# Performance work log

Measured on AMD Instinct MI355X. Metric: run time of the kernel, lower is better.

## Reference

```python
import jax, jax.numpy as jnp
import numpy as np

H = 8          # num_head
HD = 64        # head_dim = hidden_dim // num_head
WIN = 33       # atten_window_size (odd)
MIN_SCORE = -1e9


def setup_inputs() -> dict:
    key = jax.random.key(0)
    ks = jax.random.split(key, 12)
    B, S, D = 8, 4096, 512
    scale = 1.0 / np.sqrt(D).astype(np.float32)

    def lin_w(k):
        return jax.random.normal(k, (D, D), jnp.float32) * scale

    return {
        "query": jax.random.normal(ks[0], (B, S, D), jnp.float32),
        "key": jax.random.normal(ks[1], (B, S, D), jnp.float32),
        "value": jax.random.normal(ks[2], (B, S, D), jnp.float32),
        "mask": jax.random.randint(ks[3], (B, S), 0, 2).astype(bool),
        "Wq": lin_w(ks[4]), "bq": jax.random.normal(ks[5], (D,), jnp.float32) * 0.02,
        "Wk": lin_w(ks[6]), "bk": jax.random.normal(ks[7], (D,), jnp.float32) * 0.02,
        "Wv": lin_w(ks[8]), "bv": jax.random.normal(ks[9], (D,), jnp.float32) * 0.02,
        "Wo": lin_w(ks[10]), "bo": jax.random.normal(ks[11], (D,), jnp.float32) * 0.02,
    }


def reference(query, key, value, mask, Wq, bq, Wk, bk, Wv, bv, Wo, bo):
    B, S, D = query.shape
    half = min(WIN // 2, S // 2)

    def proj_split(x, W, b):
        # nn.Linear: x @ W.T + b; then split heads and flatten (B,H) -> B*H
        y = x @ W.T + b
        return y.reshape(B, S, H, HD).transpose(0, 2, 1, 3).reshape(B * H, S, HD)

    q = proj_split(query, Wq, bq)   # [BH, S, HD]
    k = proj_split(key, Wk, bk)
    v = proj_split(value, Wv, bv)
    # mask expanded over heads; True = masked (LocalAttention semantics)
    m = jnp.broadcast_to(mask[:, None, :], (B, H, S)).reshape(B * H, S)

    # banded scores: one [BH, S] vector per window offset (no sqrt(head_dim) scaling,
    # faithful to LocalAttention)
    scores = []
    for off in range(-half, half + 1):
        if off < 0:
            w = jnp.sum(q[:, -off:] * k[:, :off], axis=-1)
            w = jnp.where(m[:, :off], MIN_SCORE, w)
            w = jnp.pad(w, ((0, 0), (-off, 0)), constant_values=MIN_SCORE)
        elif off == 0:
            w = jnp.where(m, MIN_SCORE, jnp.sum(q * k, axis=-1))
        else:
            w = jnp.sum(q[:, :-off] * k[:, off:], axis=-1)
            w = jnp.where(m[:, off:], MIN_SCORE, w)
            w = jnp.pad(w, ((0, 0), (0, off)), constant_values=MIN_SCORE)
        scores.append(w)
    probs = jax.nn.softmax(jnp.stack(scores, axis=-1), axis=-1)  # [BH, S, 2*half+1]

    # weighted gather of values along the band (dropout=0 -> identity)
    out = jnp.zeros_like(v)
    for i, off in enumerate(range(-half, half + 1)):
        p = probs[:, :, i:i + 1]
        if off < 0:
            out = out + jnp.pad(p[:, -off:] * v[:, :off], ((0, 0), (-off, 0), (0, 0)))
        elif off == 0:
            out = out + p * v
        else:
            out = out + jnp.pad(p[:, :-off] * v[:, off:], ((0, 0), (0, off), (0, 0)))

    out = out.reshape(B, H, S, HD).transpose(0, 2, 1, 3).reshape(B, S, D)
    return out @ Wo.T + bo
```

## Files before the change

### kernel.cpp

```cpp
#include <hip/hip_runtime.h>
#include <hip/hip_bf16.h>
#include <stdint.h>

#define BB 8
#define SS 4096
#define DD 512
#define HH 8
#define HDIM 64

typedef unsigned short u16;
typedef __attribute__((ext_vector_type(4))) float f32x4;
typedef __attribute__((ext_vector_type(4))) short s16x4;
typedef __attribute__((ext_vector_type(8))) short s16x8;
typedef __attribute__((ext_vector_type(4))) unsigned int u32x4;

__device__ __forceinline__ u16 f2bf(float f) {
  uint32_t x = __builtin_bit_cast(uint32_t, f);
  x += 0x7fffu + ((x >> 16) & 1u);
  return (u16)(x >> 16);
}
__device__ __forceinline__ float bf2f(u16 u) {
  uint32_t x = (uint32_t)u << 16;
  return __builtin_bit_cast(float, x);
}
__device__ __forceinline__ uint32_t cvtpk(float a, float b) {
  uint32_t d;
  asm("v_cvt_pk_bf16_f32 %0, %1, %2" : "=v"(d) : "v"(a), "v"(b));
  return d;
}

__device__ __forceinline__ void gld_lds16(const void* g, void* l) {
  __builtin_amdgcn_global_load_lds((const __attribute__((address_space(1))) void*)g,
                                   (__attribute__((address_space(3))) void*)l, 16, 0, 0);
}

__device__ __forceinline__ s16x4 ld_u16x4(const u16* p) {
  const uint32_t a = *(const uint32_t*)(p);
  const uint32_t b = *(const uint32_t*)(p + 2);
  s16x4 r;
  r[0] = (short)(a & 0xffff); r[1] = (short)(a >> 16);
  r[2] = (short)(b & 0xffff); r[3] = (short)(b >> 16);
  return r;
}

__global__ void cvt_f32_bf16(const float* __restrict__ in, u16* __restrict__ out, int n8) {
  int i = blockIdx.x * blockDim.x + threadIdx.x;
  const int stride = gridDim.x * blockDim.x;
  for (; i < n8; i += stride) {
    const f32x4 a0 = *(const f32x4*)(in + (size_t)i * 8);
    const f32x4 a1 = *(const f32x4*)(in + (size_t)i * 8 + 4);
    s16x8 pk;
#pragma unroll
    for (int j = 0; j < 4; ++j) pk[j] = (short)f2bf(a0[j]);
#pragma unroll
    for (int j = 0; j < 4; ++j) pk[4 + j] = (short)f2bf(a1[j]);
    *(s16x8*)(out + (size_t)i * 8) = pk;
  }
}

__global__ void cvt_weights(const float* __restrict__ w0, const float* __restrict__ w1,
                            const float* __restrict__ w2, const float* __restrict__ w3,
                            u16* __restrict__ out) {
  int i = blockIdx.x * blockDim.x + threadIdx.x;
  const int n = DD * DD;
  if (i < n) {
    out[i]         = f2bf(w0[i]);
    out[n + i]     = f2bf(w1[i]);
    out[2 * n + i] = f2bf(w2[i]);
    out[3 * n + i] = f2bf(w3[i]);
  }
}

__global__ void mask_unpack(const void* __restrict__ mraw, uint8_t* __restrict__ mk, int n) {
  __shared__ int bad[3];
  __shared__ int mode;
  const int t = threadIdx.x;
  if (t < 3) bad[t] = 0;
  __syncthreads();
  const uint32_t* w = (const uint32_t*)mraw;
  const uint32_t x = w[t];
  const bool w01 = (x == 0u) || (x == 1u);
  const uint32_t ob = x | (x >> 8) | (x >> 16) | (x >> 24);
  const bool u01 = ((ob & 0xFEu) == 0u);
  if (!w01) atomicAdd(&bad[0], 1);
  if (!u01) atomicAdd(&bad[1], 1);
  __syncthreads();
  if (t == 0) mode = (bad[0] == 0) ? 0 : (bad[1] == 0 ? 1 : 2);
  __syncthreads();
  const int md = mode;
  for (int i = blockIdx.x * 256 + t; i < n; i += gridDim.x * 256) {
    uint8_t v;
    if (md == 0)      v = (uint8_t)(w[i] & 1u);
    else if (md == 1) v = ((const uint8_t*)mraw)[i] ? 1 : 0;
    else              v = (w[i] != 0u) ? 1 : 0;
    mk[i] = v;
  }
}

template <typename TC>
__global__ __launch_bounds__(256, 2)
void gemm_f32a(const float* __restrict__ A, const u16* __restrict__ Bw,
               const float* __restrict__ bias, TC* __restrict__ C,
               int M, int N, int K) {
  __shared__ __align__(16) u16 sA[2][128 * 64];
  __shared__ __align__(16) u16 sB[2][128 * 64];

  const int tid = threadIdx.x;
  const int lane = tid & 63, wv = tid >> 6;
  const int wr = (wv >> 1) * 64, wc = (wv & 1) * 64;
  const int c = lane & 15, g = lane >> 4;
  const int lid = blockIdx.x;
  const int rb = (lid >> 5) * 8 + (lid & 7);
  const int cb = (lid >> 3) & 3;
  const int col0 = cb * 128, row0 = rb * 128;

  const int srB = tid >> 3, cBc = (tid & 7) ^ ((tid >> 3) & 7);
  const u16* b_src = Bw + (size_t)(col0 + srB) * K + cBc * 8;
  auto stageB = [&](int buf, int ko) {
#pragma unroll
    for (int i = 0; i < 4; ++i)
      gld_lds16(b_src + (size_t)i * 32 * K + ko, (char*)sB[buf] + i * 4096 + wv * 1024);
  };

  const int art = tid >> 3, ajt = tid & 7;
  const float* a_src = A + (size_t)(row0 + art) * K + ajt * 8;
  f32x4 aR[4][2];
  auto loadA = [&](int ko) {
#pragma unroll
    for (int i = 0; i < 4; ++i) {
      const float* p = a_src + (size_t)(i * 32) * K + ko;
      aR[i][0] = *(const f32x4*)p;
      aR[i][1] = *(const f32x4*)(p + 4);
    }
  };
  auto writeA = [&](int buf) {
#pragma unroll
    for (int i = 0; i < 4; ++i) {
      const int row = art + i * 32;
      const u32x4 dd = (u32x4){cvtpk(aR[i][0][0], aR[i][0][1]), cvtpk(aR[i][0][2], aR[i][0][3]),
                               cvtpk(aR[i][1][0], aR[i][1][1]), cvtpk(aR[i][1][2], aR[i][1][3])};
      *(s16x8*)&sA[buf][row * 64 + ((ajt ^ (row & 7)) * 8)] = __builtin_bit_cast(s16x8, dd);
    }
  };

  f32x4 acc[4][4];
#pragma unroll
  for (int a = 0; a < 4; ++a)
#pragma unroll
    for (int b = 0; b < 4; ++b) acc[a][b] = (f32x4){0.f, 0.f, 0.f, 0.f};

  const int nkt = K / 64;
  loadA(0);
  stageB(0, 0);
  writeA(0);
  __syncthreads();
  int cur = 0;
  for (int kt = 0; kt < nkt; ++kt) {
    if (kt + 1 < nkt) {
      loadA((kt + 1) * 64);
      stageB(cur ^ 1, (kt + 1) * 64);
    }

#pragma unroll
    for (int ks = 0; ks < 2; ++ks) {
      s16x8 af[4], bq[4];
#pragma unroll
      for (int mf = 0; mf < 4; ++mf) {
        const int row = wr + mf * 16 + c;
        af[mf] = *(const s16x8*)&sA[cur][row * 64 + (((ks * 4 + g) ^ (c & 7)) * 8)];
      }
#pragma unroll
      for (int nf = 0; nf < 4; ++nf) {
        const int row = wc + nf * 16 + c;
        bq[nf] = *(const s16x8*)&sB[cur][row * 64 + (((ks * 4 + g) ^ (c & 7)) * 8)];
      }
#pragma unroll
      for (int mf = 0; mf < 4; ++mf)
#pragma unroll
        for (int nf = 0; nf < 4; ++nf)
          acc[mf][nf] = __builtin_amdgcn_mfma_f32_16x16x32_bf16(af[mf], bq[nf], acc[mf][nf], 0, 0, 0);
    }
    if (kt + 1 < nkt) writeA(cur ^ 1);
    __syncthreads();
    cur ^= 1;
  }

#pragma unroll
  for (int nf = 0; nf < 4; ++nf) {
    const int col = col0 + wc + nf * 16 + c;
    const float bv = bias[col];
#pragma unroll
    for (int mf = 0; mf < 4; ++mf) {
#pragma unroll
      for (int i = 0; i < 4; ++i) {
        const int row = row0 + wr + mf * 16 + g * 4 + i;
        const float v = acc[mf][nf][i] + bv;
        if constexpr (sizeof(TC) == 4) C[(size_t)row * N + col] = v;
        else                           C[(size_t)row * N + col] = (TC)f2bf(v);
      }
    }
  }
}

template <typename TC>
__global__ __launch_bounds__(256, 2)
void gemm_db(const u16* __restrict__ A, const u16* __restrict__ Bw,
             const float* __restrict__ bias, TC* __restrict__ C,
             int M, int N, int K) {
  __shared__ __align__(16) u16 sA[2][128 * 64];
  __shared__ __align__(16) u16 sB[2][128 * 64];

  const int tid = threadIdx.x;
  const int lane = tid & 63, wv = tid >> 6;
  const int wr = (wv >> 1) * 64, wc = (wv & 1) * 64;
  const int c = lane & 15, g = lane >> 4;
  const int lid = blockIdx.x;
  const int rb = (lid >> 5) * 8 + (lid & 7);
  const int cb = (lid >> 3) & 3;
  const int col0 = cb * 128, row0 = rb * 128;

  const int srB = tid >> 3, cBc = (tid & 7) ^ ((tid >> 3) & 7);
  const u16* a_src = A + (size_t)(row0 + srB) * K + cBc * 8;
  const u16* b_src = Bw + (size_t)(col0 + srB) * K + cBc * 8;

  auto stage = [&](int buf, int ko) {
#pragma unroll
    for (int i = 0; i < 4; ++i)
      gld_lds16(a_src + (size_t)i * 32 * K + ko, (char*)sA[buf] + i * 4096 + wv * 1024);
#pragma unroll
    for (int i = 0; i < 4; ++i)
      gld_lds16(b_src + (size_t)i * 32 * K + ko, (char*)sB[buf] + i * 4096 + wv * 1024);
  };

  f32x4 acc[4][4];
#pragma unroll
  for (int a = 0; a < 4; ++a)
#pragma unroll
    for (int b = 0; b < 4; ++b) acc[a][b] = (f32x4){0.f, 0.f, 0.f, 0.f};

  const int nkt = K / 64;
  stage(0, 0);
  __syncthreads();
  int cur = 0;
  for (int kt = 0; kt < nkt; ++kt) {
    if (kt + 1 < nkt) stage(cur ^ 1, (kt + 1) * 64);

#pragma unroll
    for (int ks = 0; ks < 2; ++ks) {
      s16x8 af[4], bq[4];
#pragma unroll
      for (int mf = 0; mf < 4; ++mf) {
        const int row = wr + mf * 16 + c;
        af[mf] = *(const s16x8*)&sA[cur][row * 64 + (((ks * 4 + g) ^ (c & 7)) * 8)];
      }
#pragma unroll
      for (int nf = 0; nf < 4; ++nf) {
        const int row = wc + nf * 16 + c;
        bq[nf] = *(const s16x8*)&sB[cur][row * 64 + (((ks * 4 + g) ^ (c & 7)) * 8)];
      }
#pragma unroll
      for (int mf = 0; mf < 4; ++mf)
#pragma unroll
        for (int nf = 0; nf < 4; ++nf)
          acc[mf][nf] = __builtin_amdgcn_mfma_f32_16x16x32_bf16(af[mf], bq[nf], acc[mf][nf], 0, 0, 0);
    }
    __syncthreads();
    cur ^= 1;
  }

#pragma unroll
  for (int nf = 0; nf < 4; ++nf) {
    const int col = col0 + wc + nf * 16 + c;
    const float bv = bias[col];
#pragma unroll
    for (int mf = 0; mf < 4; ++mf) {
#pragma unroll
      for (int i = 0; i < 4; ++i) {
        const int row = row0 + wr + mf * 16 + g * 4 + i;
        const float v = acc[mf][nf][i] + bv;
        if constexpr (sizeof(TC) == 4) C[(size_t)row * N + col] = v;
        else                           C[(size_t)row * N + col] = (TC)f2bf(v);
      }
    }
  }
}

__device__ __forceinline__ void hilo8(const f32x4& a0, const f32x4& a1, s16x8& h, s16x8& l) {
#pragma unroll
  for (int j = 0; j < 4; ++j) {
    const float f = a0[j];
    const u16 hb = f2bf(f);
    h[j] = (short)hb;
    l[j] = (short)f2bf(f - bf2f(hb));
  }
#pragma unroll
  for (int j = 0; j < 4; ++j) {
    const float f = a1[j];
    const u16 hb = f2bf(f);
    h[4 + j] = (short)hb;
    l[4 + j] = (short)f2bf(f - bf2f(hb));
  }
}

#define ACH 4
#define VSTR 98

__global__ __launch_bounds__(256, 4)
void attn_mfma(const float* __restrict__ Qp, const float* __restrict__ Kp,
               const u16* __restrict__ Vp, const uint8_t* __restrict__ mk,
               u16* __restrict__ O) {
  __shared__ u16 sKh[96 * 72];
  __shared__ u16 sKl[96 * 68];
  __shared__ u16 sVT[64 * VSTR];
  __shared__ u16 sM[96];

  const int bh = blockIdx.x;
  const int b = bh >> 3, h = bh & 7;
  const int base0 = blockIdx.y * (64 * ACH);
  const int tid = threadIdx.x;

  const int wv = tid >> 6, lane = tid & 63;
  const int c = lane & 15, g = lane >> 4;
  const int qloc = wv * 16 + c;
  const int kb = wv * 16;

  const int krow0 = tid >> 3, kj = tid & 7;
  const int kks = kj >> 2, kg2 = kj & 3;
  const int vk0 = tid >> 3, vdg8 = tid & 7;

  f32x4 kA0[3], kA1[3];
  s16x8 vR[3];
  u16 mR = 1;
  f32x4 qn0[2], qn1[2];

  auto issue_loads = [&](int cs) {
#pragma unroll
    for (int it = 0; it < 3; ++it) {
      const int row = krow0 + it * 32;
      const int gr = cs - 16 + row;
      if (gr >= 0 && gr < SS) {
        const float* kp = Kp + ((size_t)(b * SS + gr)) * DD + h * HDIM + kks * 32 + kg2 * 4;
        kA0[it] = *(const f32x4*)kp;
        kA1[it] = *(const f32x4*)(kp + 16);
      } else {
        kA0[it] = (f32x4){0.f, 0.f, 0.f, 0.f};
        kA1[it] = (f32x4){0.f, 0.f, 0.f, 0.f};
      }
    }
#pragma unroll
    for (int it = 0; it < 3; ++it) {
      const int k = vk0 + it * 32;
      const int gr = cs - 16 + k;
      if (gr >= 0 && gr < SS)
        vR[it] = *(const s16x8*)(Vp + ((size_t)(b * SS + gr)) * DD + h * HDIM + vdg8 * 8);
      else
        vR[it] = (s16x8){0, 0, 0, 0, 0, 0, 0, 0};
    }
    if (tid < 96) {
      const int gr = cs - 16 + tid;
      mR = (gr < 0 || gr >= SS || mk[b * SS + gr]) ? 1 : 0;
    }
    const float* qp = Qp + ((size_t)(b * SS + cs + qloc)) * DD + h * HDIM;
#pragma unroll
    for (int ks = 0; ks < 2; ++ks) {
      qn0[ks] = *(const f32x4*)(qp + 32 * ks + 4 * g);
      qn1[ks] = *(const f32x4*)(qp + 32 * ks + 16 + 4 * g);
    }
  };

  auto write_stage = [&]() {
#pragma unroll
    for (int it = 0; it < 3; ++it) {
      const int row = krow0 + it * 32;
      s16x8 hh, ll;
      hilo8(kA0[it], kA1[it], hh, ll);
      *(s16x8*)&sKh[row * 72 + kj * 8] = hh;
      *(s16x4*)&sKl[row * 68 + kj * 8]     = (s16x4){ll[0], ll[1], ll[2], ll[3]};
      *(s16x4*)&sKl[row * 68 + kj * 8 + 4] = (s16x4){ll[4], ll[5], ll[6], ll[7]};
    }
#pragma unroll
    for (int it = 0; it < 3; ++it) {
      const int k = vk0 + it * 32;
#pragma unroll
      for (int i = 0; i < 8; ++i)
        sVT[(vdg8 * 8 + i) * VSTR + k] = (u16)vR[it][i];
    }
    if (tid < 96) sM[tid] = mR;
  };

  issue_loads(base0);
  write_stage();
  __syncthreads();

  for (int t = 0; t < ACH; ++t) {
    const int s0 = base0 + t * 64;
    const int qrow = s0 + qloc;

    s16x8 qh[2], qlo[2];
#pragma unroll
    for (int ks = 0; ks < 2; ++ks) hilo8(qn0[ks], qn1[ks], qh[ks], qlo[ks]);

    if (t + 1 < ACH) issue_loads(base0 + (t + 1) * 64);

    f32x4 st[3];
#pragma unroll
    for (int kt = 0; kt < 3; ++kt) st[kt] = (f32x4){0.f, 0.f, 0.f, 0.f};
    __builtin_amdgcn_s_setprio(1);
#pragma unroll
    for (int kt = 0; kt < 3; ++kt) {
      const int krow = kb + kt * 16 + c;
      const int rb72 = krow * 72;
      const int rb68 = krow * 68;
#pragma unroll
      for (int ks = 0; ks < 2; ++ks) {
        const s16x8 kh = *(const s16x8*)&sKh[rb72 + ks * 32 + g * 8];
        const s16x4 l0 = *(const s16x4*)&sKl[rb68 + ks * 32 + g * 8];
        const s16x4 l1 = *(const s16x4*)&sKl[rb68 + ks * 32 + g * 8 + 4];
        const s16x8 kl = (s16x8){l0[0], l0[1], l0[2], l0[3], l1[0], l1[1], l1[2], l1[3]};
        st[kt] = __builtin_amdgcn_mfma_f32_16x16x32_bf16(kh, qh[ks], st[kt], 0, 0, 0);
        st[kt] = __builtin_amdgcn_mfma_f32_16x16x32_bf16(kh, qlo[ks], st[kt], 0, 0, 0);
        st[kt] = __builtin_amdgcn_mfma_f32_16x16x32_bf16(kl, qh[ks], st[kt], 0, 0, 0);
      }
    }
    __builtin_amdgcn_s_setprio(0);

    float mx = -3.0e9f;
#pragma unroll
    for (int kt = 0; kt < 3; ++kt) {
#pragma unroll
      for (int i = 0; i < 4; ++i) {
        const int delta = kt * 16 + 4 * g + i - 16 - c;
        const int key = kb + kt * 16 + 4 * g + i;
        float v;
        if (delta < -16 || delta > 16) v = -2.0e9f;
        else if (sM[key])              v = -1.0e9f;
        else                           v = st[kt][i];
        st[kt][i] = v;
        mx = fmaxf(mx, v);
      }
    }
    mx = fmaxf(mx, __shfl_xor(mx, 16));
    mx = fmaxf(mx, __shfl_xor(mx, 32));
    float sum = 0.f;
#pragma unroll
    for (int kt = 0; kt < 3; ++kt) {
#pragma unroll
      for (int i = 0; i < 4; ++i) {
        const float e = __expf(st[kt][i] - mx);
        st[kt][i] = e;
        sum += e;
      }
    }
    sum += __shfl_xor(sum, 16);
    sum += __shfl_xor(sum, 32);
    const float inv = 1.f / sum;

    s16x8 ph[2];
#pragma unroll
    for (int i = 0; i < 4; ++i) {
      ph[0][i]     = (short)f2bf(st[0][i]);
      ph[0][4 + i] = (short)f2bf(st[1][i]);
      ph[1][i]     = (short)f2bf(st[2][i]);
      ph[1][4 + i] = 0;
    }

    f32x4 ot[4];
#pragma unroll
    for (int dt = 0; dt < 4; ++dt) ot[dt] = (f32x4){0.f, 0.f, 0.f, 0.f};
    __builtin_amdgcn_s_setprio(1);
#pragma unroll
    for (int dt = 0; dt < 4; ++dt) {
      const int rowb = (dt * 16 + c) * VSTR;
      const s16x4 v0 = ld_u16x4(&sVT[rowb + kb + 4 * g]);
      const s16x4 v1 = ld_u16x4(&sVT[rowb + kb + 16 + 4 * g]);
      const s16x8 vh0 = (s16x8){v0[0], v0[1], v0[2], v0[3], v1[0], v1[1], v1[2], v1[3]};
      ot[dt] = __builtin_amdgcn_mfma_f32_16x16x32_bf16(vh0, ph[0], ot[dt], 0, 0, 0);
      const s16x4 v2 = ld_u16x4(&sVT[rowb + kb + 32 + 4 * g]);
      const s16x8 vh1 = (s16x8){v2[0], v2[1], v2[2], v2[3], 0, 0, 0, 0};
      ot[dt] = __builtin_amdgcn_mfma_f32_16x16x32_bf16(vh1, ph[1], ot[dt], 0, 0, 0);
    }
    __builtin_amdgcn_s_setprio(0);

    u16* op = O + ((size_t)(b * SS + qrow)) * DD + h * HDIM;
#pragma unroll
    for (int dt = 0; dt < 4; ++dt) {
      s16x4 pk;
#pragma unroll
      for (int i = 0; i < 4; ++i) pk[i] = (short)f2bf(ot[dt][i] * inv);
      *(s16x4*)&op[dt * 16 + 4 * g] = pk;
    }

    __syncthreads();
    if (t + 1 < ACH) {
      write_stage();
      __syncthreads();
    }
  }
}

__global__ __launch_bounds__(256)
void attn_win(const u16* __restrict__ Qp, const u16* __restrict__ Kp,
              const u16* __restrict__ Vp, const uint8_t* __restrict__ mk,
              u16* __restrict__ O) {
  constexpr int KR = 96;
  __shared__ float sK[KR][HDIM];
  __shared__ float sV[KR][HDIM];
  __shared__ float sMf[KR];

  const int bh = blockIdx.x;
  const int b = bh >> 3, h = bh & 7;
  const int s0 = blockIdx.y * 64;
  const int tid = threadIdx.x;

  for (int c = tid; c < KR * 16; c += 256) {
    const int row = c >> 4, c4 = c & 15;
    const int gr = s0 - 16 + row;
    float kv[4], vv[4];
    if (gr >= 0 && gr < SS) {
      const size_t base = ((size_t)(b * SS + gr)) * DD + h * HDIM + c4 * 4;
      const s16x4 kk = *(const s16x4*)(Kp + base);
      const s16x4 vx = *(const s16x4*)(Vp + base);
#pragma unroll
      for (int i = 0; i < 4; ++i) { kv[i] = bf2f((u16)kk[i]); vv[i] = bf2f((u16)vx[i]); }
    } else {
#pragma unroll
      for (int i = 0; i < 4; ++i) { kv[i] = 0.f; vv[i] = 0.f; }
    }
#pragma unroll
    for (int i = 0; i < 4; ++i) {
      const int d = c4 * 4 + i;
      const int pd = (d & 15) * 4 + (d >> 4);
      sK[row][pd] = kv[i];
      sV[row][pd] = vv[i];
    }
  }
  for (int r = tid; r < KR; r += 256) {
    const int gr = s0 - 16 + r;
    sMf[r] = (gr < 0 || gr >= SS || mk[b * SS + gr]) ? 1.f : 0.f;
  }
  __syncthreads();

  const int wv = tid >> 6, lane = tid & 63;
  const int g = lane >> 4, d16 = lane & 15;

  for (int rr = 0; rr < 16; rr += 4) {
    const int lr = wv * 16 + rr + g;
    const int srow = s0 + lr;
    const u16* qp = Qp + ((size_t)(b * SS + srow)) * DD + h * HDIM;
    float q0 = bf2f(qp[d16]), q1 = bf2f(qp[d16 + 16]), q2 = bf2f(qp[d16 + 32]), q3 = bf2f(qp[d16 + 48]);
    float sc[33];
#pragma unroll
    for (int o = 0; o < 33; ++o) {
      const f32x4 kk = *(const f32x4*)&sK[lr + o][d16 * 4];
      float p = q0 * kk[0] + q1 * kk[1] + q2 * kk[2] + q3 * kk[3];
      p += __shfl_xor(p, 1);
      p += __shfl_xor(p, 2);
      p += __shfl_xor(p, 4);
      p += __shfl_xor(p, 8);
      sc[o] = (sMf[lr + o] != 0.f) ? -1.0e9f : p;
    }
    float mx = sc[0];
#pragma unroll
    for (int o = 1; o < 33; ++o) mx = fmaxf(mx, sc[o]);
    float sum = 0.f;
#pragma unroll
    for (int o = 0; o < 33; ++o) { const float e = __expf(sc[o] - mx); sc[o] = e; sum += e; }
    const float inv = 1.f / sum;
    f32x4 acc = (f32x4){0.f, 0.f, 0.f, 0.f};
#pragma unroll
    for (int o = 0; o < 33; ++o) {
      const f32x4 vx = *(const f32x4*)&sV[lr + o][d16 * 4];
      acc += (sc[o] * inv) * vx;
    }
    u16* op = O + ((size_t)(b * SS + srow)) * DD + h * HDIM;
    op[d16]      = f2bf(acc[0]);
    op[d16 + 16] = f2bf(acc[1]);
    op[d16 + 32] = f2bf(acc[2]);
    op[d16 + 48] = f2bf(acc[3]);
  }
}

extern "C" void kernel_launch(void* const* d_in, const int* in_sizes, int n_in,
                              void* d_out, int out_size, void* d_ws, size_t ws_size,
                              hipStream_t stream) {
  const float* query = (const float*)d_in[0];
  const float* key   = (const float*)d_in[1];
  const float* value = (const float*)d_in[2];
  const void*  mraw  = d_in[3];
  const float* Wq = (const float*)d_in[4];
  const float* bq = (const float*)d_in[5];
  const float* Wk = (const float*)d_in[6];
  const float* bk = (const float*)d_in[7];
  const float* Wv = (const float*)d_in[8];
  const float* bv = (const float*)d_in[9];
  const float* Wo = (const float*)d_in[10];
  const float* bo = (const float*)d_in[11];

  const int M = BB * SS, N = DD, K = DD;

  char* ws = (char*)d_ws;
  size_t off = 0;
  auto carve = [&](size_t bytes) -> char* {
    char* p = ws + off;
    off = (off + bytes + 255) & ~(size_t)255;
    return p;
  };
  u16* wAll   = (u16*)carve((size_t)4 * DD * DD * sizeof(u16));
  uint8_t* mk = (uint8_t*)carve((size_t)BB * SS);

  const size_t qk_f32 = (size_t)M * DD * 4;
  const size_t v_b16  = (size_t)M * DD * 2;
  const bool f32p = (off + 2 * qk_f32 + 2 * v_b16 + 1024) <= ws_size;

  cvt_weights<<<(DD * DD + 255) / 256, 256, 0, stream>>>(Wq, Wk, Wv, Wo, wAll);
  mask_unpack<<<16, 256, 0, stream>>>(mraw, mk, BB * SS);

  const dim3 gg((M / 128) * (N / 128));
  const dim3 ga(BB * HH, SS / (64 * ACH));

  if (f32p) {
    float* Qf = (float*)carve(qk_f32);
    float* Kf = (float*)carve(qk_f32);
    u16*   Vb = (u16*)carve(v_b16);
    u16*   AO = (u16*)carve(v_b16);
    gemm_f32a<float><<<gg, 256, 0, stream>>>(query, wAll,               bq, Qf, M, N, K);
    gemm_f32a<float><<<gg, 256, 0, stream>>>(key,   wAll + DD * DD,     bk, Kf, M, N, K);
    gemm_f32a<u16><<<gg, 256, 0, stream>>>(value, wAll + 2 * DD * DD, bv, Vb, M, N, K);
    attn_mfma<<<ga, 256, 0, stream>>>(Qf, Kf, Vb, mk, AO);
    gemm_db<float><<<gg, 256, 0, stream>>>(AO, wAll + 3 * DD * DD, bo, (float*)d_out, M, N, K);
  } else {
    const dim3 ga1(BB * HH, SS / 64);
    const int n8 = M * DD / 8;
    const dim3 gc(2048);
    u16* Xb = (u16*)carve(v_b16);
    u16* Qb = (u16*)carve(v_b16);
    u16* Kb = (u16*)carve(v_b16);
    u16* Vb = (u16*)carve(v_b16);
    u16* AO = Xb;
    cvt_f32_bf16<<<gc, 256, 0, stream>>>(query, Xb, n8);
    gemm_db<u16><<<gg, 256, 0, stream>>>(Xb, wAll,               bq, Qb, M, N, K);
    cvt_f32_bf16<<<gc, 256, 0, stream>>>(key, Xb, n8);
    gemm_db<u16><<<gg, 256, 0, stream>>>(Xb, wAll + DD * DD,     bk, Kb, M, N, K);
    cvt_f32_bf16<<<gc, 256, 0, stream>>>(value, Xb, n8);
    gemm_db<u16><<<gg, 256, 0, stream>>>(Xb, wAll + 2 * DD * DD, bv, Vb, M, N, K);
    attn_win<<<ga1, 256, 0, stream>>>(Qb, Kb, Vb, mk, AO);
    gemm_db<float><<<gg, 256, 0, stream>>>(AO, wAll + 3 * DD * DD, bo, (float*)d_out, M, N, K);
  }
}
```

Measured before the change: 221.0 us.

## Merge Q/K/V projection GEMMs into one launch and deepen A prefetch

Replaces three separate f32-input projection GEMM launches with a single grid of three times the blocks, where each block picks its input, weight, bias and output from its block index. It also reorders the K-loop so the A tile for step k+1 is written to LDS before the MFMA work and the global load for step k+2 is issued early, giving a two-deep register prefetch. This aims to cut launch overhead and tail effects and to hide global load latency better, at the cost of more live registers and runtime branches in the epilogue.

Result: slower. 229.7 us (+3.9%).

```diff
diff --git a/kernel.cpp b/kernel.cpp
--- a/kernel.cpp
+++ b/kernel.cpp
@@ -97,11 +97,13 @@
   }
 }
 
-template <typename TC>
 __global__ __launch_bounds__(256, 2)
-void gemm_f32a(const float* __restrict__ A, const u16* __restrict__ Bw,
-               const float* __restrict__ bias, TC* __restrict__ C,
-               int M, int N, int K) {
+void gemm_qkv(const float* __restrict__ Aq, const float* __restrict__ Ak,
+              const float* __restrict__ Av, const u16* __restrict__ wAll,
+              const float* __restrict__ bq, const float* __restrict__ bk,
+              const float* __restrict__ bv,
+              float* __restrict__ Qf, float* __restrict__ Kf, u16* __restrict__ Vb,
+              int M, int N, int K) {
   __shared__ __align__(16) u16 sA[2][128 * 64];
   __shared__ __align__(16) u16 sB[2][128 * 64];
 
@@ -110,9 +112,15 @@
   const int wr = (wv >> 1) * 64, wc = (wv & 1) * 64;
   const int c = lane & 15, g = lane >> 4;
   const int lid = blockIdx.x;
-  const int rb = (lid >> 5) * 8 + (lid & 7);
-  const int cb = (lid >> 3) & 3;
+  const int which = lid >> 10;
+  const int sub = lid & 1023;
+  const int rb = (sub >> 5) * 8 + (sub & 7);
+  const int cb = (sub >> 3) & 3;
   const int col0 = cb * 128, row0 = rb * 128;
+
+  const float* A    = (which == 0) ? Aq : (which == 1 ? Ak : Av);
+  const u16*   Bw   = wAll + which * DD * DD;
+  const float* bias = (which == 0) ? bq : (which == 1 ? bk : bv);
 
   const int srB = tid >> 3, cBc = (tid & 7) ^ ((tid >> 3) & 7);
   const u16* b_src = Bw + (size_t)(col0 + srB) * K + cBc * 8;
@@ -153,17 +161,19 @@
   loadA(0);
   stageB(0, 0);
   writeA(0);
+  loadA(64);
   __syncthreads();
   int cur = 0;
   for (int kt = 0; kt < nkt; ++kt) {
     if (kt + 1 < nkt) {
-      loadA((kt + 1) * 64);
+      writeA(cur ^ 1);
       stageB(cur ^ 1, (kt + 1) * 64);
     }
+    if (kt + 2 < nkt) loadA((kt + 2) * 64);
 
 #pragma unroll
     for (int ks = 0; ks < 2; ++ks) {
-      s16x8 af[4], bq[4];
+      s16x8 af[4], bq4[4];
 #pragma unroll
       for (int mf = 0; mf < 4; ++mf) {
         const int row = wr + mf * 16 + c;
@@ -172,15 +182,14 @@
 #pragma unroll
       for (int nf = 0; nf < 4; ++nf) {
         const int row = wc + nf * 16 + c;
-        bq[nf] = *(const s16x8*)&sB[cur][row * 64 + (((ks * 4 + g) ^ (c & 7)) * 8)];
+        bq4[nf] = *(const s16x8*)&sB[cur][row * 64 + (((ks * 4 + g) ^ (c & 7)) * 8)];
       }
 #pragma unroll
       for (int mf = 0; mf < 4; ++mf)
 #pragma unroll
         for (int nf = 0; nf < 4; ++nf)
-          acc[mf][nf] = __builtin_amdgcn_mfma_f32_16x16x32_bf16(af[mf], bq[nf], acc[mf][nf], 0, 0, 0);
-    }
-    if (kt + 1 < nkt) writeA(cur ^ 1);
+          acc[mf][nf] = __builtin_amdgcn_mfma_f32_16x16x32_bf16(af[mf], bq4[nf], acc[mf][nf], 0, 0, 0);
+    }
     __syncthreads();
     cur ^= 1;
   }
@@ -188,15 +197,16 @@
 #pragma unroll
   for (int nf = 0; nf < 4; ++nf) {
     const int col = col0 + wc + nf * 16 + c;
-    const float bv = bias[col];
+    const float bvv = bias[col];
 #pragma unroll
     for (int mf = 0; mf < 4; ++mf) {
 #pragma unroll
       for (int i = 0; i < 4; ++i) {
         const int row = row0 + wr + mf * 16 + g * 4 + i;
-        const float v = acc[mf][nf][i] + bv;
-        if constexpr (sizeof(TC) == 4) C[(size_t)row * N + col] = v;
-        else                           C[(size_t)row * N + col] = (TC)f2bf(v);
+        const float v = acc[mf][nf][i] + bvv;
+        if (which == 2) Vb[(size_t)row * N + col] = f2bf(v);
+        else if (which == 0) Qf[(size_t)row * N + col] = v;
+        else Kf[(size_t)row * N + col] = v;
       }
     }
   }
@@ -623,9 +633,8 @@
     float* Kf = (float*)carve(qk_f32);
     u16*   Vb = (u16*)carve(v_b16);
     u16*   AO = (u16*)carve(v_b16);
-    gemm_f32a<float><<<gg, 256, 0, stream>>>(query, wAll,               bq, Qf, M, N, K);
-    gemm_f32a<float><<<gg, 256, 0, stream>>>(key,   wAll + DD * DD,     bk, Kf, M, N, K);
-    gemm_f32a<u16><<<gg, 256, 0, stream>>>(value, wAll + 2 * DD * DD, bv, Vb, M, N, K);
+    gemm_qkv<<<dim3(3 * 1024), 256, 0, stream>>>(query, key, value, wAll,
+                                                 bq, bk, bv, Qf, Kf, Vb, M, N, K);
     attn_mfma<<<ga, 256, 0, stream>>>(Qf, Kf, Vb, mk, AO);
     gemm_db<float><<<gg, 256, 0, stream>>>(AO, wAll + 3 * DD * DD, bo, (float*)d_out, M, N, K);
   } else {
```

## Halve GEMM K-tile, use plane-major LDS layout, prefetch A two tiles ahead

Applied to the files above, without the earlier changes.

The f32-input projection GEMM now uses a K-step of 32 instead of 64. This halves shared memory per block, and the launch bound is raised to 4 blocks per CU. LDS is reorganised into four 8-element K-planes with an XOR swizzle, and the fp32 A tile is now loaded two iterations ahead and converted to bf16 before the next stage. The aim is more occupancy and better hiding of global load latency. The cost is twice as many barriers per K loop and tighter register limits, which could cause spills.

New measurement: 236.8 us. +7.1%, slower.

```diff
diff --git a/kernel.cpp b/kernel.cpp
--- a/kernel.cpp
+++ b/kernel.cpp
@@ -98,12 +98,12 @@
 }
 
 template <typename TC>
-__global__ __launch_bounds__(256, 2)
+__global__ __launch_bounds__(256, 4)
 void gemm_f32a(const float* __restrict__ A, const u16* __restrict__ Bw,
                const float* __restrict__ bias, TC* __restrict__ C,
                int M, int N, int K) {
-  __shared__ __align__(16) u16 sA[2][128 * 64];
-  __shared__ __align__(16) u16 sB[2][128 * 64];
+  __shared__ __align__(16) u16 sA[2][128 * 32];
+  __shared__ __align__(16) u16 sB[2][128 * 32];
 
   const int tid = threadIdx.x;
   const int lane = tid & 63, wv = tid >> 6;
@@ -114,33 +114,30 @@
   const int cb = (lid >> 3) & 3;
   const int col0 = cb * 128, row0 = rb * 128;
 
-  const int srB = tid >> 3, cBc = (tid & 7) ^ ((tid >> 3) & 7);
-  const u16* b_src = Bw + (size_t)(col0 + srB) * K + cBc * 8;
+  const int bRow = tid & 127;
+  const int bPl  = tid >> 7;
+  const u16* b_src0 = Bw + (size_t)(col0 + bRow) * K + (((0 * 2 + bPl) ^ (bRow & 3)) * 8);
+  const u16* b_src1 = Bw + (size_t)(col0 + bRow) * K + (((1 * 2 + bPl) ^ (bRow & 3)) * 8);
   auto stageB = [&](int buf, int ko) {
-#pragma unroll
-    for (int i = 0; i < 4; ++i)
-      gld_lds16(b_src + (size_t)i * 32 * K + ko, (char*)sB[buf] + i * 4096 + wv * 1024);
+    gld_lds16(b_src0 + ko, (char*)sB[buf] + 0 * 4096 + wv * 1024);
+    gld_lds16(b_src1 + ko, (char*)sB[buf] + 1 * 4096 + wv * 1024);
   };
 
-  const int art = tid >> 3, ajt = tid & 7;
-  const float* a_src = A + (size_t)(row0 + art) * K + ajt * 8;
-  f32x4 aR[4][2];
+  const int aRow = tid >> 1, aH = tid & 1;
+  const float* a_src = A + (size_t)(row0 + aRow) * K + aH * 16;
+  f32x4 aR[4];
   auto loadA = [&](int ko) {
 #pragma unroll
-    for (int i = 0; i < 4; ++i) {
-      const float* p = a_src + (size_t)(i * 32) * K + ko;
-      aR[i][0] = *(const f32x4*)p;
-      aR[i][1] = *(const f32x4*)(p + 4);
-    }
+    for (int q = 0; q < 4; ++q) aR[q] = *(const f32x4*)(a_src + ko + q * 4);
   };
   auto writeA = [&](int buf) {
-#pragma unroll
-    for (int i = 0; i < 4; ++i) {
-      const int row = art + i * 32;
-      const u32x4 dd = (u32x4){cvtpk(aR[i][0][0], aR[i][0][1]), cvtpk(aR[i][0][2], aR[i][0][3]),
-                               cvtpk(aR[i][1][0], aR[i][1][1]), cvtpk(aR[i][1][2], aR[i][1][3])};
-      *(s16x8*)&sA[buf][row * 64 + ((ajt ^ (row & 7)) * 8)] = __builtin_bit_cast(s16x8, dd);
-    }
+    const int j0 = aH * 2, j1 = aH * 2 + 1;
+    const u32x4 d0 = (u32x4){cvtpk(aR[0][0], aR[0][1]), cvtpk(aR[0][2], aR[0][3]),
+                             cvtpk(aR[1][0], aR[1][1]), cvtpk(aR[1][2], aR[1][3])};
+    const u32x4 d1 = (u32x4){cvtpk(aR[2][0], aR[2][1]), cvtpk(aR[2][2], aR[2][3]),
+                             cvtpk(aR[3][0], aR[3][1]), cvtpk(aR[3][2], aR[3][3])};
+    *(s16x8*)&sA[buf][((j0 ^ (aRow & 3)) * 1024) + aRow * 8] = __builtin_bit_cast(s16x8, d0);
+    *(s16x8*)&sA[buf][((j1 ^ (aRow & 3)) * 1024) + aRow * 8] = __builtin_bit_cast(s16x8, d1);
   };
 
   f32x4 acc[4][4];
@@ -149,38 +146,37 @@
 #pragma unroll
     for (int b = 0; b < 4; ++b) acc[a][b] = (f32x4){0.f, 0.f, 0.f, 0.f};
 
-  const int nkt = K / 64;
+  const int nkt = K / 32;
   loadA(0);
   stageB(0, 0);
   writeA(0);
+  loadA(32);
   __syncthreads();
   int cur = 0;
   for (int kt = 0; kt < nkt; ++kt) {
     if (kt + 1 < nkt) {
-      loadA((kt + 1) * 64);
-      stageB(cur ^ 1, (kt + 1) * 64);
-    }
-
-#pragma unroll
-    for (int ks = 0; ks < 2; ++ks) {
-      s16x8 af[4], bq[4];
-#pragma unroll
-      for (int mf = 0; mf < 4; ++mf) {
-        const int row = wr + mf * 16 + c;
-        af[mf] = *(const s16x8*)&sA[cur][row * 64 + (((ks * 4 + g) ^ (c & 7)) * 8)];
-      }
-#pragma unroll
-      for (int nf = 0; nf < 4; ++nf) {
-        const int row = wc + nf * 16 + c;
-        bq[nf] = *(const s16x8*)&sB[cur][row * 64 + (((ks * 4 + g) ^ (c & 7)) * 8)];
-      }
-#pragma unroll
-      for (int mf = 0; mf < 4; ++mf)
-#pragma unroll
-        for (int nf = 0; nf < 4; ++nf)
-          acc[mf][nf] = __builtin_amdgcn_mfma_f32_16x16x32_bf16(af[mf], bq[nf], acc[mf][nf], 0, 0, 0);
-    }
-    if (kt + 1 < nkt) writeA(cur ^ 1);
+      writeA(cur ^ 1);
+      stageB(cur ^ 1, (kt + 1) * 32);
+    }
+    if (kt + 2 < nkt) loadA((kt + 2) * 32);
+
+    s16x8 af[4], bq[4];
+#pragma unroll
+    for (int mf = 0; mf < 4; ++mf) {
+      const int row = wr + mf * 16 + c;
+      af[mf] = *(const s16x8*)&sA[cur][((g ^ (c & 3)) * 1024) + row * 8];
+    }
+#pragma unroll
+    for (int nf = 0; nf < 4; ++nf) {
+      const int row = wc + nf * 16 + c;
+      bq[nf] = *(const s16x8*)&sB[cur][((g ^ (c & 3)) * 1024) + row * 8];
+    }
+#pragma unroll
+    for (int mf = 0; mf < 4; ++mf)
+#pragma unroll
+      for (int nf = 0; nf < 4; ++nf)
+        acc[mf][nf] = __builtin_amdgcn_mfma_f32_16x16x32_bf16(af[mf], bq[nf], acc[mf][nf], 0, 0, 0);
+
     __syncthreads();
     cur ^= 1;
   }
```
